# Kernel tuning notes

Measured on AMD Instinct MI355X. Metric: run time of the kernel, lower is better.

Reference implementation:

```python
import jax, jax.numpy as jnp
import numpy as np

B, D, H, C = 512, 1024, 512, 4


def setup_inputs() -> dict:
    key = jax.random.key(0)
    k_x, k_v, k_w = jax.random.split(key, 3)
    # x holds categorical values in [0, C) used as float multipliers
    x = jax.random.randint(k_x, (B, D), 0, C).astype(jnp.float32)
    # xavier_normal_ per torch fan computation: V fan_in=D*C, fan_out=H*C; W fan_in=D, fan_out=H
    V = jax.random.normal(k_v, (H, D, C), jnp.float32) * np.float32(np.sqrt(2.0 / (D * C + H * C)))
    b = jnp.zeros((D, C), jnp.float32)
    W = jax.random.normal(k_w, (H, D), jnp.float32) * np.float32(np.sqrt(2.0 / (D + H)))
    c = jnp.zeros((1, H), jnp.float32)
    return {"x": x, "V": V, "b": b, "W": W, "c": c}


def _nade_forward(x, V, b, W, c):
    Bsz = x.shape[0]
    a0 = jnp.broadcast_to(c, (Bsz, c.shape[1]))  # [B, H]
    # per-step slices stacked along leading D axis for lax.scan
    xs = (jnp.transpose(V, (1, 0, 2)),  # [D, H, C]
          b,                            # [D, C]
          W.T,                          # [D, H]
          x.T)                          # [D, B]

    def step(a, inp):
        V_d, b_d, w_d, x_d = inp
        h = jax.nn.sigmoid(a)                 # [B, H]
        logits = h @ V_d + b_d                # [B, C]
        p = jax.nn.log_softmax(logits, axis=1)
        a_new = a + x_d[:, None] * w_d[None, :]  # rank-1 update of running preactivation
        return a_new, (logits, p)

    _, (logits, p) = jax.lax.scan(step, a0, xs)   # each [D, B, C]
    y_hat = jnp.transpose(logits, (1, 0, 2)).reshape(Bsz, -1)  # [B, D*C], d-major blocks of size C
    p_hat = jnp.transpose(p, (1, 0, 2)).reshape(Bsz, -1)
    return y_hat, p_hat


def reference(x, V, b, W, c):
    return _nade_forward(x, V, b, W, c)
```

## Files before the change

kernel.cpp:

```cpp
#include <hip/hip_runtime.h>


#define Bv 512
#define Dv 1024
#define Hv 512
#define Cv 4
#define Kv 32
#define DCv 32

#define L2E 1.4426950408889634f
#define LN2 0.6931471805599453f

typedef __attribute__((ext_vector_type(8))) short short8;
typedef __attribute__((ext_vector_type(4))) float f32x4;
typedef __attribute__((ext_vector_type(2))) float v2f;

__device__ __forceinline__ float fexp2(float x) { return __builtin_amdgcn_exp2f(x); }
__device__ __forceinline__ float flog2(float x) { return __builtin_amdgcn_logf(x); }
__device__ __forceinline__ float frcp(float x)  { return __builtin_amdgcn_rcpf(x); }

__device__ __forceinline__ v2f fma2(v2f a, v2f b, v2f c) {
#if __has_builtin(__builtin_elementwise_fma)
    return __builtin_elementwise_fma(a, b, c);
#else
    v2f r; r.x = fmaf(a.x, b.x, c.x); r.y = fmaf(a.y, b.y, c.y); return r;
#endif
}

__device__ __forceinline__ unsigned bf16pk(float lo, float hi) {
    return __builtin_amdgcn_perm(__float_as_uint(hi), __float_as_uint(lo), 0x07060302u);
}
__device__ __forceinline__ unsigned short bf16rne(float f) {
    unsigned u = __float_as_uint(f);
    return (unsigned short)((u + 0x7FFFu + ((u >> 16) & 1u)) >> 16);
}

__global__ __launch_bounds__(256) void k_prep_all(
        const float* __restrict__ V, const float* __restrict__ W,
        const float* __restrict__ x, unsigned short* __restrict__ VtA4,
        float* __restrict__ WtL, float* __restrict__ xt) {
    __shared__ char smem[17408];
    const int bid = blockIdx.x;
    if (bid < 256) {
        unsigned short* tile = (unsigned short*)smem;
        const int d0 = bid * 4;
        const int dd = threadIdx.x & 3;
        const int hb0 = threadIdx.x >> 2;
#pragma unroll
        for (int p = 0; p < 8; ++p) {
            int h = p * 64 + hb0;
            float4 v = *(const float4*)(V + ((size_t)h * Dv + d0 + dd) * Cv);
            int hb = h >> 5, q = (h >> 3) & 3, j = h & 7;
            int base = ((dd * 16 + hb) * 16 + q * 4) * 8 + j;
            tile[base + 0]  = bf16rne(v.x);
            tile[base + 8]  = bf16rne(v.y);
            tile[base + 16] = bf16rne(v.z);
            tile[base + 24] = bf16rne(v.w);
        }
        __syncthreads();
        uint4* dst = (uint4*)(VtA4 + (size_t)d0 * 2048);
        const uint4* src = (const uint4*)tile;
        for (int t = threadIdx.x; t < 1024; t += 256) dst[t] = src[t];
    } else {
        float (*t)[65] = (float (*)[65])smem;
        const int mb   = (bid - 256) >> 7;
        const int tile = (bid - 256) & 127;
        const int tr   = tile >> 4;
        const int tc   = tile & 15;
        const float* src = mb ? x : W;
        float* dst       = mb ? xt : WtL;
        const float scale = mb ? 1.0f : L2E;
        const int lx = threadIdx.x & 15;
        const int ly = threadIdx.x >> 4;
#pragma unroll
        for (int r = 0; r < 64; r += 16) {
            int row = r + ly;
            float4 v = *(const float4*)(src + (size_t)(tr * 64 + row) * Dv + tc * 64 + lx * 4);
            t[row][lx * 4 + 0] = v.x;
            t[row][lx * 4 + 1] = v.y;
            t[row][lx * 4 + 2] = v.z;
            t[row][lx * 4 + 3] = v.w;
        }
        __syncthreads();
#pragma unroll
        for (int r = 0; r < 64; r += 16) {
            int row = r + ly;
            float4 o = make_float4(t[lx * 4 + 0][row] * scale,
                                   t[lx * 4 + 1][row] * scale,
                                   t[lx * 4 + 2][row] * scale,
                                   t[lx * 4 + 3][row] * scale);
            *(float4*)(dst + (size_t)(tc * 64 + row) * 512 + tr * 64 + lx * 4) = o;
        }
    }
}

__global__ __launch_bounds__(512) void k_state(
        const float* __restrict__ x, const float* __restrict__ WtL,
        const float* __restrict__ cb, float* __restrict__ A0) {
    __shared__ float xs[Dv * 2];
    const int bg = blockIdx.x;
    const int h  = threadIdx.x;
#pragma unroll
    for (int p = 0; p < 4; ++p) {
        int idx = p * 512 + threadIdx.x;
        int g = idx >> 10;
        int d = idx & (Dv - 1);
        xs[d * 2 + g] = x[(size_t)(bg * 2 + g) * Dv + d];
    }
    __syncthreads();
    float cl = cb[h] * L2E;
    v2f run = {cl, cl};
    const float* wp = WtL + h;
    for (int kk = 0; kk < Kv; ++kk) {
        float* a0p = A0 + ((size_t)kk * Bv + bg * 2) * Hv + h;
        a0p[0]  = run.x;
        a0p[Hv] = run.y;
        const float* wkk = wp + (size_t)kk * DCv * Hv;
        const v2f* xk = (const v2f*)(xs + kk * DCv * 2);
#pragma unroll 8
        for (int j = 0; j < DCv; ++j) {
            float wv = wkk[(size_t)j * Hv];
            run = fma2(xk[j], (v2f){wv, wv}, run);
        }
    }
}

__global__ __launch_bounds__(128) void k_main(
        const float* __restrict__ xt, const float* __restrict__ bbias,
        const unsigned short* __restrict__ VtA4, const float* __restrict__ WtL,
        const float* __restrict__ A0, float* __restrict__ out) {
    const int k    = blockIdx.x >> 5;
    const int bg   = blockIdx.x & 31;
    const int wv   = threadIdx.x >> 6;
    const int lane = threadIdx.x & 63;
    const int bl   = lane & 15;
    const int quad = lane >> 4;
    const int b    = bg * 16 + bl;
    const int d0   = k * DCv;

    __shared__ f32x4 red[2][2][2][64];

    v2f a2[32];
    {
        const float* ap = A0 + ((size_t)k * Bv + b) * Hv + wv * 256 + quad * 8;
#pragma unroll
        for (int kb = 0; kb < 8; ++kb)
#pragma unroll
            for (int t = 0; t < 4; ++t)
                a2[kb * 4 + t] = *(const v2f*)(ap + kb * 32 + 2 * t);
    }

    const int blc = (bl < 4) ? bl : 0;
    const unsigned short* vp = VtA4 + (((size_t)d0 * 16 + wv * 8) * 16 + quad * 4 + blc) * 8;
    const float* wp = WtL + (size_t)d0 * Hv + wv * 256 + quad * 8;
    const float* xp = xt + (size_t)d0 * Bv + b;
    const float* bp = bbias + (d0 + wv) * Cv;
    float* sy = out + (size_t)b * Dv * Cv + (d0 + wv) * Cv;
    float* spp = sy + (size_t)Bv * Dv * Cv;

    for (int i1 = 0; i1 < DCv / 2; ++i1) {
        float xdA = xp[0];
        float xdB = xp[Bv];
        float4 bbv = *(const float4*)bp;

        f32x4 accA = {0.f, 0.f, 0.f, 0.f};
#pragma unroll
        for (int kb = 0; kb < 8; ++kb) {
            union { unsigned u[4]; short8 s; } cv;
#pragma unroll
            for (int t = 0; t < 4; ++t) {
                v2f aa = a2[kb * 4 + t];
                v2f e; e.x = fexp2(-aa.x); e.y = fexp2(-aa.y);
                v2f q = e + 1.0f;
                cv.u[t] = bf16pk(frcp(q.x), frcp(q.y));
            }
            short8 af = *(const short8*)(vp + kb * 128);
            accA = __builtin_amdgcn_mfma_f32_16x16x32_bf16(af, cv.s, accA, 0, 0, 0);
        }
        v2f xA2 = {xdA, xdA};
#pragma unroll
        for (int kb = 0; kb < 8; ++kb)
#pragma unroll
            for (int t = 0; t < 4; ++t)
                a2[kb * 4 + t] = fma2(xA2, *(const v2f*)(wp + kb * 32 + 2 * t), a2[kb * 4 + t]);

        f32x4 accB = {0.f, 0.f, 0.f, 0.f};
#pragma unroll
        for (int kb = 0; kb < 8; ++kb) {
            union { unsigned u[4]; short8 s; } cv;
#pragma unroll
            for (int t = 0; t < 4; ++t) {
                v2f aa = a2[kb * 4 + t];
                v2f e; e.x = fexp2(-aa.x); e.y = fexp2(-aa.y);
                v2f q = e + 1.0f;
                cv.u[t] = bf16pk(frcp(q.x), frcp(q.y));
            }
            short8 af = *(const short8*)(vp + 2048 + kb * 128);
            accB = __builtin_amdgcn_mfma_f32_16x16x32_bf16(af, cv.s, accB, 0, 0, 0);
        }
        v2f xB2 = {xdB, xdB};
#pragma unroll
        for (int kb = 0; kb < 8; ++kb)
#pragma unroll
            for (int t = 0; t < 4; ++t)
                a2[kb * 4 + t] = fma2(xB2, *(const v2f*)(wp + Hv + kb * 32 + 2 * t), a2[kb * 4 + t]);

        red[i1 & 1][0][wv][lane] = accA;
        red[i1 & 1][1][wv][lane] = accB;
        __syncthreads();

        f32x4 s = red[i1 & 1][wv][0][lane] + red[i1 & 1][wv][1][lane];
        float w0 = s.x + bbv.x;
        float w1 = s.y + bbv.y;
        float w2 = s.z + bbv.z;
        float w3 = s.w + bbv.w;
        float mx = fmaxf(fmaxf(w0, w1), fmaxf(w2, w3));
        float e0 = fexp2((w0 - mx) * L2E);
        float e1 = fexp2((w1 - mx) * L2E);
        float e2 = fexp2((w2 - mx) * L2E);
        float e3 = fexp2((w3 - mx) * L2E);
        float lse = mx + flog2(e0 + e1 + e2 + e3) * LN2;
        if (quad == 0) {
            *(float4*)sy  = make_float4(w0, w1, w2, w3);
            *(float4*)spp = make_float4(w0 - lse, w1 - lse, w2 - lse, w3 - lse);
        }

        vp += 2 * 2048;
        wp += 2 * Hv;
        xp += 2 * Bv;
        bp += 2 * Cv;
        sy += 2 * Cv;
        spp += 2 * Cv;
    }
}

extern "C" void kernel_launch(void* const* d_in, const int* in_sizes, int n_in,
                              void* d_out, int out_size, void* d_ws, size_t ws_size,
                              hipStream_t stream) {
    const float* x  = (const float*)d_in[0];
    const float* V  = (const float*)d_in[1];
    const float* bb = (const float*)d_in[2];
    const float* W  = (const float*)d_in[3];
    const float* cb = (const float*)d_in[4];
    float* out = (float*)d_out;

    char* ws = (char*)d_ws;
    unsigned short* VtA4 = (unsigned short*)ws;
    float* WtL = (float*)(ws + (size_t)4 * 1024 * 1024);
    float* xt  = (float*)(ws + (size_t)6 * 1024 * 1024);
    float* A0  = (float*)(ws + (size_t)8 * 1024 * 1024);

    k_prep_all<<<512, 256, 0, stream>>>(V, W, x, VtA4, WtL, xt);
    k_state<<<Bv / 2, 512, 0, stream>>>(x, WtL, cb, A0);
    k_main<<<Kv * 32, 128, 0, stream>>>(xt, bb, VtA4, WtL, A0, out);
}
```

Measured before the change: 194.0 us.

## Parallelize chunk-start state via partial sums plus prefix scan, store in fp16

```diff
diff --git a/kernel.cpp b/kernel.cpp
--- a/kernel.cpp
+++ b/kernel.cpp
@@ -1,12 +1,13 @@
 #include <hip/hip_runtime.h>
+#include <hip/hip_fp16.h>
 
 
 #define Bv 512
 #define Dv 1024
 #define Hv 512
 #define Cv 4
-#define Kv 32
-#define DCv 32
+#define Kv 64
+#define DCv 16
 
 #define L2E 1.4426950408889634f
 #define LN2 0.6931471805599453f
@@ -94,41 +95,63 @@
     }
 }
 
-__global__ __launch_bounds__(512) void k_state(
-        const float* __restrict__ x, const float* __restrict__ WtL,
-        const float* __restrict__ cb, float* __restrict__ A0) {
-    __shared__ float xs[Dv * 2];
-    const int bg = blockIdx.x;
-    const int h  = threadIdx.x;
-#pragma unroll
-    for (int p = 0; p < 4; ++p) {
-        int idx = p * 512 + threadIdx.x;
-        int g = idx >> 10;
-        int d = idx & (Dv - 1);
-        xs[d * 2 + g] = x[(size_t)(bg * 2 + g) * Dv + d];
+__global__ __launch_bounds__(512) void k_partial(const float* __restrict__ x,
+                          const float* __restrict__ WtL, __half* __restrict__ P) {
+    int k  = blockIdx.x >> 6;
+    int bg = blockIdx.x & 63;
+    int h  = threadIdx.x;
+    int d0 = k * DCv;
+
+    __shared__ float xs[DCv * 8];
+    if (threadIdx.x < DCv * 8) {
+        int g = threadIdx.x & 7;
+        int j = threadIdx.x >> 3;
+        xs[j * 8 + g] = x[(size_t)(bg * 8 + g) * Dv + d0 + j];
     }
     __syncthreads();
-    float cl = cb[h] * L2E;
-    v2f run = {cl, cl};
-    const float* wp = WtL + h;
-    for (int kk = 0; kk < Kv; ++kk) {
-        float* a0p = A0 + ((size_t)kk * Bv + bg * 2) * Hv + h;
-        a0p[0]  = run.x;
-        a0p[Hv] = run.y;
-        const float* wkk = wp + (size_t)kk * DCv * Hv;
-        const v2f* xk = (const v2f*)(xs + kk * DCv * 2);
-#pragma unroll 8
-        for (int j = 0; j < DCv; ++j) {
-            float wv = wkk[(size_t)j * Hv];
-            run = fma2(xk[j], (v2f){wv, wv}, run);
-        }
+
+    float acc[8];
+#pragma unroll
+    for (int g = 0; g < 8; ++g) acc[g] = 0.0f;
+
+    const float* wp = WtL + (size_t)d0 * Hv + h;
+#pragma unroll
+    for (int j = 0; j < DCv; ++j) {
+        float wv = wp[(size_t)j * Hv];
+        const float4 x0 = *(const float4*)(xs + j * 8);
+        const float4 x1 = *(const float4*)(xs + j * 8 + 4);
+        acc[0] = fmaf(x0.x, wv, acc[0]);
+        acc[1] = fmaf(x0.y, wv, acc[1]);
+        acc[2] = fmaf(x0.z, wv, acc[2]);
+        acc[3] = fmaf(x0.w, wv, acc[3]);
+        acc[4] = fmaf(x1.x, wv, acc[4]);
+        acc[5] = fmaf(x1.y, wv, acc[5]);
+        acc[6] = fmaf(x1.z, wv, acc[6]);
+        acc[7] = fmaf(x1.w, wv, acc[7]);
+    }
+#pragma unroll
+    for (int g = 0; g < 8; ++g)
+        P[((size_t)k * Bv + bg * 8 + g) * Hv + h] = __float2half(acc[g]);
+}
+
+__global__ void k_prefix(__half* __restrict__ A0, const float* __restrict__ cbias) {
+    int gid = blockIdx.x * blockDim.x + threadIdx.x;
+    int h = gid & (Hv - 1);
+    int bi = gid >> 9;
+    float run = cbias[h] * L2E;
+    __half* p = A0 + (size_t)bi * Hv + h;
+#pragma unroll 4
+    for (int k = 0; k < Kv; ++k) {
+        float t = __half2float(p[(size_t)k * Bv * Hv]);
+        p[(size_t)k * Bv * Hv] = __float2half(run);
+        run += t;
     }
 }
 
 __global__ __launch_bounds__(128) void k_main(
         const float* __restrict__ xt, const float* __restrict__ bbias,
         const unsigned short* __restrict__ VtA4, const float* __restrict__ WtL,
-        const float* __restrict__ A0, float* __restrict__ out) {
+        const __half* __restrict__ A0, float* __restrict__ out) {
     const int k    = blockIdx.x >> 5;
     const int bg   = blockIdx.x & 31;
     const int wv   = threadIdx.x >> 6;
@@ -142,12 +165,17 @@
 
     v2f a2[32];
     {
-        const float* ap = A0 + ((size_t)k * Bv + b) * Hv + wv * 256 + quad * 8;
-#pragma unroll
-        for (int kb = 0; kb < 8; ++kb)
-#pragma unroll
-            for (int t = 0; t < 4; ++t)
-                a2[kb * 4 + t] = *(const v2f*)(ap + kb * 32 + 2 * t);
+        const __half* ap = A0 + ((size_t)k * Bv + b) * Hv + wv * 256 + quad * 8;
+#pragma unroll
+        for (int kb = 0; kb < 8; ++kb) {
+            union { uint4 u; __half2 h2[4]; } t;
+            t.u = *(const uint4*)(ap + kb * 32);
+#pragma unroll
+            for (int tt = 0; tt < 4; ++tt) {
+                float2 f = __half22float2(t.h2[tt]);
+                a2[kb * 4 + tt] = (v2f){f.x, f.y};
+            }
+        }
     }
 
     const int blc = (bl < 4) ? bl : 0;
@@ -179,10 +207,14 @@
         }
         v2f xA2 = {xdA, xdA};
 #pragma unroll
-        for (int kb = 0; kb < 8; ++kb)
-#pragma unroll
-            for (int t = 0; t < 4; ++t)
-                a2[kb * 4 + t] = fma2(xA2, *(const v2f*)(wp + kb * 32 + 2 * t), a2[kb * 4 + t]);
+        for (int kb = 0; kb < 8; ++kb) {
+            float4 w0 = *(const float4*)(wp + kb * 32);
+            float4 w1 = *(const float4*)(wp + kb * 32 + 4);
+            a2[kb*4+0] = fma2(xA2, (v2f){w0.x, w0.y}, a2[kb*4+0]);
+            a2[kb*4+1] = fma2(xA2, (v2f){w0.z, w0.w}, a2[kb*4+1]);
+            a2[kb*4+2] = fma2(xA2, (v2f){w1.x, w1.y}, a2[kb*4+2]);
+            a2[kb*4+3] = fma2(xA2, (v2f){w1.z, w1.w}, a2[kb*4+3]);
+        }
 
         f32x4 accB = {0.f, 0.f, 0.f, 0.f};
 #pragma unroll
@@ -200,10 +232,14 @@
         }
         v2f xB2 = {xdB, xdB};
 #pragma unroll
-        for (int kb = 0; kb < 8; ++kb)
-#pragma unroll
-            for (int t = 0; t < 4; ++t)
-                a2[kb * 4 + t] = fma2(xB2, *(const v2f*)(wp + Hv + kb * 32 + 2 * t), a2[kb * 4 + t]);
+        for (int kb = 0; kb < 8; ++kb) {
+            float4 w0 = *(const float4*)(wp + Hv + kb * 32);
+            float4 w1 = *(const float4*)(wp + Hv + kb * 32 + 4);
+            a2[kb*4+0] = fma2(xB2, (v2f){w0.x, w0.y}, a2[kb*4+0]);
+            a2[kb*4+1] = fma2(xB2, (v2f){w0.z, w0.w}, a2[kb*4+1]);
+            a2[kb*4+2] = fma2(xB2, (v2f){w1.x, w1.y}, a2[kb*4+2]);
+            a2[kb*4+3] = fma2(xB2, (v2f){w1.z, w1.w}, a2[kb*4+3]);
+        }
 
         red[i1 & 1][0][wv][lane] = accA;
         red[i1 & 1][1][wv][lane] = accB;
@@ -248,9 +284,10 @@
     unsigned short* VtA4 = (unsigned short*)ws;
     float* WtL = (float*)(ws + (size_t)4 * 1024 * 1024);
     float* xt  = (float*)(ws + (size_t)6 * 1024 * 1024);
-    float* A0  = (float*)(ws + (size_t)8 * 1024 * 1024);
+    __half* A0 = (__half*)(ws + (size_t)8 * 1024 * 1024);
 
     k_prep_all<<<512, 256, 0, stream>>>(V, W, x, VtA4, WtL, xt);
-    k_state<<<Bv / 2, 512, 0, stream>>>(x, WtL, cb, A0);
+    k_partial<<<Kv * (Bv / 8), 512, 0, stream>>>(x, WtL, A0);
+    k_prefix<<<(Bv * Hv) / 256, 256, 0, stream>>>(A0, cb);
     k_main<<<Kv * 32, 128, 0, stream>>>(xt, bb, VtA4, WtL, A0, out);
 }
```

New measurement: 175.4 us. 9.6% less time.
